# Kernel tuning notes

Hardware: AMD Instinct MI355X
Metric: run time of the kernel (lower is better)

The kernel has to match this reference:

```python
import jax, jax.numpy as jnp
import numpy as np
import math

DIM = 4096
DV = 1024          # compress_dim
H = 16             # num_heads
NS = 32            # num_seeds
B, L = 8, 2048
EPS = 1e-5


def _layernorm(x, g, b):
    mu = jnp.mean(x, axis=-1, keepdims=True)
    var = jnp.mean((x - mu) ** 2, axis=-1, keepdims=True)
    return (x - mu) * jax.lax.rsqrt(var + EPS) * g + b


def setup_inputs() -> dict:
    key = jax.random.key(0)
    ks = jax.random.split(key, 12)
    def lin(k, out_d, in_d):
        scale = math.sqrt(6.0 / (in_d + out_d))  # xavier_uniform
        return jax.random.uniform(k, (out_d, in_d), jnp.float32, -scale, scale)
    return {
        "X": jax.random.normal(ks[0], (B, L, DIM), jnp.float32),
        "pad_mask": jax.random.randint(ks[1], (B, L), 0, 2, jnp.int32),
        "S": jax.random.uniform(ks[2], (1, NS, DV), jnp.float32, -0.05, 0.05),
        "Wq": lin(ks[3], DV, DV), "bq": jnp.zeros((DV,), jnp.float32),
        "Wk": lin(ks[4], DV, DIM), "bk": jnp.zeros((DV,), jnp.float32),
        "Wv": lin(ks[5], DV, DIM), "bv": jnp.zeros((DV,), jnp.float32),
        "Wo": lin(ks[6], DV, DV), "bo": jnp.zeros((DV,), jnp.float32),
        "g0": jnp.ones((DV,), jnp.float32), "beta0": jnp.zeros((DV,), jnp.float32),
        "g1": jnp.ones((DV,), jnp.float32), "beta1": jnp.zeros((DV,), jnp.float32),
    }


def reference(X, pad_mask, S, Wq, bq, Wk, bk, Wv, bv, Wo, bo, g0, beta0, g1, beta1):
    b, l, _ = X.shape
    dh = DV // H
    scale = 1.0 / math.sqrt(DV)  # NOTE: full dim_V, not per-head dim
    Q = jnp.broadcast_to(S, (b, NS, DV))              # seeds repeated per batch
    Qp = (Q @ Wq.T + bq).reshape(b, NS, H, dh)
    Kp = (X @ Wk.T + bk).reshape(b, l, H, dh)
    Vp = (X @ Wv.T + bv).reshape(b, l, H, dh)
    score = jnp.einsum('bqhd,bkhd->bhqk', Qp, Kp) * scale
    m = (pad_mask != 0)[:, None, None, :]             # [b,1,1,k]
    score = jnp.where(m, score, jnp.float32(-1e12))
    A = jax.nn.softmax(score, axis=-1) * m.astype(score.dtype)  # post-softmax renorm
    O = jnp.einsum('bhqk,bkhd->bqhd', A, Vp).reshape(b, NS, DV)
    O = Q + O
    O = _layernorm(O, g0, beta0)
    O = O + jax.nn.relu(O @ Wo.T + bo)
    O = _layernorm(O, g1, beta1)
    return O
```

## Files before the change

### kernel.cpp

```cpp
#include <hip/hip_runtime.h>

#define DIMX 4096
#define DVX  1024
#define HX   16
#define DHX  64
#define NSX  32
#define BX   8
#define LX   2048
#define EPSF 1e-5f

typedef unsigned short u16;
typedef unsigned int   u32;

using bf16x8 = __attribute__((ext_vector_type(8))) __bf16;
using f32x4  = __attribute__((ext_vector_type(4))) float;

__device__ __forceinline__ float bfu(u16 u) {
    union { u32 i; float f; } c; c.i = ((u32)u) << 16; return c.f;
}
__device__ __forceinline__ u16 f2b(float f) {
    union { float f; u32 u; } c; c.f = f;
    u32 u = c.u;
    u32 r = (u + 0x7fffu + ((u >> 16) & 1u)) >> 16;
    return (u16)r;
}

__device__ __forceinline__ void async16(const u16* g, u16* l) {
    __builtin_amdgcn_global_load_lds(
        (const __attribute__((address_space(1))) void*)g,
        (__attribute__((address_space(3))) void*)l, 16, 0, 0);
}

template<bool ISF>
__device__ __forceinline__ void ld8(const void* base, size_t idx, float o[8]) {
    if (ISF) {
        const float* f = (const float*)base + idx;
        float4 a = *(const float4*)f, b = *(const float4*)(f + 4);
        o[0]=a.x; o[1]=a.y; o[2]=a.z; o[3]=a.w;
        o[4]=b.x; o[5]=b.y; o[6]=b.z; o[7]=b.w;
    } else {
        const u16* h = (const u16*)base + idx;
        uint4 v = *(const uint4*)h;
        o[0]=bfu(v.x & 0xffff); o[1]=bfu(v.x >> 16);
        o[2]=bfu(v.y & 0xffff); o[3]=bfu(v.y >> 16);
        o[4]=bfu(v.z & 0xffff); o[5]=bfu(v.z >> 16);
        o[6]=bfu(v.w & 0xffff); o[7]=bfu(v.w >> 16);
    }
}
__device__ __forceinline__ float ld1(const void* base, size_t idx, bool isf) {
    return isf ? ((const float*)base)[idx] : bfu(((const u16*)base)[idx]);
}

__global__ __launch_bounds__(256) void detect_kernel(const u16* __restrict__ X,
                                                     int* __restrict__ flag) {
    __shared__ int cnt;
    if (threadIdx.x == 0) cnt = 0;
    __syncthreads();
    int local = 0;
    for (int i = threadIdx.x; i < 8192; i += 256) {
        u32 e = ((u32)X[i] >> 7) & 0xffu;
        if (e >= 200u) local++;
    }
    atomicAdd(&cnt, local);
    __syncthreads();
    if (threadIdx.x == 0) *flag = (cnt > 32) ? 1 : 0;
}

__global__ __launch_bounds__(256) void cvt_kernel(const int* __restrict__ flag,
                                                  const float* __restrict__ src,
                                                  u16* __restrict__ dst, int ngrp) {
    if (*flag == 0) return;
    int stride = gridDim.x * 256;
    for (int i = blockIdx.x * 256 + threadIdx.x; i < ngrp; i += stride) {
        const float4* f = (const float4*)(src + (size_t)i * 8);
        float4 a = f[0], b = f[1];
        uint4 r;
        r.x = (u32)f2b(a.x) | ((u32)f2b(a.y) << 16);
        r.y = (u32)f2b(a.z) | ((u32)f2b(a.w) << 16);
        r.z = (u32)f2b(b.x) | ((u32)f2b(b.y) << 16);
        r.w = (u32)f2b(b.z) | ((u32)f2b(b.w) << 16);
        *(uint4*)(dst + (size_t)i * 8) = r;
    }
}

__global__ __launch_bounds__(256) void qp_kernel(
        const int* __restrict__ flag, const void* __restrict__ S,
        const void* __restrict__ Wq, const void* __restrict__ bq,
        float* __restrict__ Qp) {
    int wid = blockIdx.x * 4 + (threadIdx.x >> 6);
    int lane = threadIdx.x & 63;
    int q = wid >> 10, n = wid & 1023;
    bool isf = (*flag != 0);
    float p = 0.f;
    if (isf) {
        const float4* s4 = (const float4*)((const float*)S + (size_t)q * DVX);
        const float4* w4 = (const float4*)((const float*)Wq + (size_t)n * DVX);
#pragma unroll
        for (int e = 0; e < 4; e++) {
            float4 a = s4[e * 64 + lane];
            float4 b = w4[e * 64 + lane];
            p += a.x * b.x + a.y * b.y + a.z * b.z + a.w * b.w;
        }
    } else {
        const u16* srow = (const u16*)S + (size_t)q * DVX + lane * 16;
        const u16* wrow = (const u16*)Wq + (size_t)n * DVX + lane * 16;
#pragma unroll
        for (int c = 0; c < 2; c++) {
            uint4 a = *(const uint4*)(srow + c * 8);
            uint4 b = *(const uint4*)(wrow + c * 8);
            p += bfu(a.x & 0xffff) * bfu(b.x & 0xffff) + bfu(a.x >> 16) * bfu(b.x >> 16)
               + bfu(a.y & 0xffff) * bfu(b.y & 0xffff) + bfu(a.y >> 16) * bfu(b.y >> 16)
               + bfu(a.z & 0xffff) * bfu(b.z & 0xffff) + bfu(a.z >> 16) * bfu(b.z >> 16)
               + bfu(a.w & 0xffff) * bfu(b.w & 0xffff) + bfu(a.w >> 16) * bfu(b.w >> 16);
        }
    }
#pragma unroll
    for (int off = 32; off > 0; off >>= 1)
        p += __shfl_xor(p, off, 64);
    if (lane == 0) Qp[wid] = p + ld1(bq, n, isf);
}

__global__ __launch_bounds__(512, 2) void kv_gemm3(
        const int* __restrict__ flag,
        const void* __restrict__ X,  const u16* __restrict__ Xb,
        const void* __restrict__ Wk, const void* __restrict__ bk,
        const void* __restrict__ Wv, const void* __restrict__ bv,
        const u16* __restrict__ Wkb, const u16* __restrict__ Wvb,
        u16* __restrict__ Kp, u16* __restrict__ Vp) {
    extern __shared__ __align__(16) u16 lds[];
    const bool isf = (*flag != 0);
    const u16* Xs = isf ? Xb : (const u16*)X;

    const int t = threadIdx.x;
    const int lane = t & 63, w = t >> 6;
    const int wm = w >> 2, wn = w & 3;
    const int quad = lane >> 4, l16 = lane & 15;
    const int l8 = l16 & 7;

    const int bid = blockIdx.x;
    const int swz = (bid & 7) * 64 + (bid >> 3);
    const int mt = swz >> 3, nt = swz & 7;
    const int m0 = mt * 256, n0 = nt * 256;

    const u16* Wb16; const void* bias; int boff;
    if (n0 < DVX) { Wb16 = (isf ? Wkb : (const u16*)Wk) + (size_t)n0 * DIMX;
                    bias = bk; boff = n0; }
    else          { Wb16 = (isf ? Wvb : (const u16*)Wv) + (size_t)(n0 - DVX) * DIMX;
                    bias = bv; boff = n0 - DVX; }

    f32x4 acc[8][4];
#pragma unroll
    for (int i = 0; i < 8; i++)
#pragma unroll
        for (int j = 0; j < 4; j++) acc[i][j] = {0.f, 0.f, 0.f, 0.f};

    {
        u16* An = lds;
        u16* Bn = lds + 32768;
#pragma unroll
        for (int i = 0; i < 4; i++) {
            int gi = i * 512 + t;
            int r = gi >> 3;
            int g = (gi & 7) ^ (r & 7);
            async16(Xs + (size_t)(m0 + r) * DIMX + g * 8, An + gi * 8);
        }
#pragma unroll
        for (int i = 0; i < 4; i++) {
            int gi = i * 512 + t;
            int r = gi >> 3;
            int g = (gi & 7) ^ (r & 7);
            async16(Wb16 + (size_t)r * DIMX + g * 8, Bn + gi * 8);
        }
        asm volatile("s_waitcnt vmcnt(0)" ::: "memory");
        __builtin_amdgcn_s_barrier();
    }

    for (int kt = 0; kt < DIMX / 64; kt++) {
        u16* Ab = lds + (kt & 1) * 16384;
        u16* Bb = lds + 32768 + (kt & 1) * 16384;
        u16* An = lds + ((kt + 1) & 1) * 16384;
        u16* Bn = lds + 32768 + ((kt + 1) & 1) * 16384;
        const int k1 = (kt + 1) * 64;

        if (kt + 1 < DIMX / 64) {
#pragma unroll
            for (int i = 0; i < 4; i++) {
                int gi = i * 512 + t;
                int r = gi >> 3;
                int g = (gi & 7) ^ (r & 7);
                async16(Xs + (size_t)(m0 + r) * DIMX + k1 + g * 8, An + gi * 8);
            }
#pragma unroll
            for (int i = 0; i < 4; i++) {
                int gi = i * 512 + t;
                int r = gi >> 3;
                int g = (gi & 7) ^ (r & 7);
                async16(Wb16 + (size_t)r * DIMX + k1 + g * 8, Bn + gi * 8);
            }
        }
        __builtin_amdgcn_sched_barrier(0);

        bf16x8 bfr[4][2];
#pragma unroll
        for (int ni = 0; ni < 4; ni++)
#pragma unroll
            for (int ks = 0; ks < 2; ks++) {
                int R = wn * 64 + ni * 16 + l16;
                int cc = ((ks * 4 + quad) ^ l8);
                bfr[ni][ks] = *(const bf16x8*)&Bb[R * 64 + cc * 8];
            }

#pragma unroll
        for (int p = 0; p < 4; p++) {
            bf16x8 a[2][2];
#pragma unroll
            for (int dm = 0; dm < 2; dm++)
#pragma unroll
                for (int ks = 0; ks < 2; ks++) {
                    int R = wm * 128 + (2 * p + dm) * 16 + l16;
                    int cc = ((ks * 4 + quad) ^ l8);
                    a[dm][ks] = *(const bf16x8*)&Ab[R * 64 + cc * 8];
                }
            __builtin_amdgcn_s_setprio(1);
#pragma unroll
            for (int dm = 0; dm < 2; dm++)
#pragma unroll
                for (int ni = 0; ni < 4; ni++)
#pragma unroll
                    for (int ks = 0; ks < 2; ks++)
                        acc[2 * p + dm][ni] = __builtin_amdgcn_mfma_f32_16x16x32_bf16(
                            a[dm][ks], bfr[ni][ks], acc[2 * p + dm][ni], 0, 0, 0);
            __builtin_amdgcn_s_setprio(0);
        }

        __builtin_amdgcn_sched_barrier(0);
        asm volatile("s_waitcnt vmcnt(0)" ::: "memory");
        __builtin_amdgcn_s_barrier();
        __builtin_amdgcn_sched_barrier(0);
    }

    float bb[4];
#pragma unroll
    for (int ni = 0; ni < 4; ni++)
        bb[ni] = ld1(bias, (size_t)(boff + wn * 64 + ni * 16 + l16), isf);
#pragma unroll
    for (int mi = 0; mi < 8; mi++) {
#pragma unroll
        for (int ni = 0; ni < 4; ni++) {
            int colL = wn * 64 + ni * 16 + l16;
            int col = n0 + colL;
            u16* dst; int dcol;
            if (col < DVX) { dst = Kp; dcol = col; }
            else           { dst = Vp; dcol = col - DVX; }
#pragma unroll
            for (int r = 0; r < 4; r++) {
                int row = m0 + wm * 128 + mi * 16 + quad * 4 + r;
                dst[(size_t)row * DVX + dcol] = f2b(acc[mi][ni][r] + bb[ni]);
            }
        }
    }
}

#define TM 128
#define TN 128
#define BKK 32
#define LDT 32

__device__ __forceinline__ uint4 pack8(float o[8]) {
    uint4 r;
    r.x = (u32)f2b(o[0]) | ((u32)f2b(o[1]) << 16);
    r.y = (u32)f2b(o[2]) | ((u32)f2b(o[3]) << 16);
    r.z = (u32)f2b(o[4]) | ((u32)f2b(o[5]) << 16);
    r.w = (u32)f2b(o[6]) | ((u32)f2b(o[7]) << 16);
    return r;
}

__global__ __launch_bounds__(256) void kv_gemm2(
        const int* __restrict__ flag,
        const void* __restrict__ X,  const u16* __restrict__ Xb,
        const void* __restrict__ Wk, const void* __restrict__ bk,
        const void* __restrict__ Wv, const void* __restrict__ bv,
        const u16* __restrict__ Wkb, const u16* __restrict__ Wvb,
        u16* __restrict__ Kp, u16* __restrict__ Vp) {
    __shared__ u16 As[TM * LDT];
    __shared__ u16 Bs[TN * LDT];
    const bool isf = (*flag != 0);
    const u16* Xs = isf ? Xb : (const u16*)X;

    const int t = threadIdx.x;
    const int lane = t & 63, w = t >> 6;
    const int wm = w >> 1, wn = w & 1;
    const int quad = lane >> 4, l16 = lane & 15;
    const int bl = blockIdx.x;
    const int xcd = bl & 7, bq = bl >> 3;
    const int m0 = (xcd + 8 * (bq >> 4)) * TM;
    const int n0 = (bq & 15) * TN;
    const u16* Wb16; const void* bias; int boff;
    if (n0 < DVX) { Wb16 = (isf ? Wkb : (const u16*)Wk) + (size_t)n0 * DIMX;
                    bias = bk; boff = n0; }
    else          { Wb16 = (isf ? Wvb : (const u16*)Wv) + (size_t)(n0 - DVX) * DIMX;
                    bias = bv; boff = n0 - DVX; }

    f32x4 acc[4][4];
#pragma unroll
    for (int i = 0; i < 4; i++)
#pragma unroll
        for (int j = 0; j < 4; j++) acc[i][j] = {0.f, 0.f, 0.f, 0.f};

    const int srow = lane >> 2;
    const int gcol = ((lane & 3) ^ ((lane >> 3) & 3)) * 8;
    const int ph = (l16 >> 1) & 3;

    for (int k0 = 0; k0 < DIMX; k0 += BKK) {
        __syncthreads();
#pragma unroll
        for (int c = 0; c < 2; c++) {
            int rr = w * 32 + c * 16;
            async16(Xs + (size_t)(m0 + rr + srow) * DIMX + k0 + gcol,
                    As + rr * LDT);
            async16(Wb16 + (size_t)(rr + srow) * DIMX + k0 + gcol,
                    Bs + rr * LDT);
        }
        __syncthreads();
        bf16x8 af[4], bfr[4];
#pragma unroll
        for (int mi = 0; mi < 4; mi++) {
            int ar = wm * 64 + mi * 16 + l16;
            af[mi] = *(const bf16x8*)&As[ar * LDT + (quad ^ ph) * 8];
        }
#pragma unroll
        for (int ni = 0; ni < 4; ni++) {
            int br = wn * 64 + ni * 16 + l16;
            bfr[ni] = *(const bf16x8*)&Bs[br * LDT + (quad ^ ph) * 8];
        }
#pragma unroll
        for (int mi = 0; mi < 4; mi++)
#pragma unroll
            for (int ni = 0; ni < 4; ni++)
                acc[mi][ni] = __builtin_amdgcn_mfma_f32_16x16x32_bf16(
                    af[mi], bfr[ni], acc[mi][ni], 0, 0, 0);
    }

#pragma unroll
    for (int mi = 0; mi < 4; mi++) {
#pragma unroll
        for (int ni = 0; ni < 4; ni++) {
            int colL = wn * 64 + ni * 16 + l16;
            int col = n0 + colL;
            float bb = ld1(bias, (size_t)(boff + colL), isf);
            u16* dst; int dcol;
            if (col < DVX) { dst = Kp; dcol = col; }
            else           { dst = Vp; dcol = col - DVX; }
#pragma unroll
            for (int r = 0; r < 4; r++) {
                int row = m0 + wm * 64 + mi * 16 + quad * 4 + r;
                dst[(size_t)row * DVX + dcol] = f2b(acc[mi][ni][r] + bb);
            }
        }
    }
}

template<bool ISF>
__device__ void kv_body(const void* __restrict__ X,
                        const void* __restrict__ Wk, const void* __restrict__ bk,
                        const void* __restrict__ Wv, const void* __restrict__ bv,
                        u16* __restrict__ Kp, u16* __restrict__ Vp,
                        u16* As, u16* Bs) {
    const int t = threadIdx.x;
    const int lane = t & 63, w = t >> 6;
    const int wm = w >> 1, wn = w & 1;
    const int quad = lane >> 4, l16 = lane & 15;
    const int bl = blockIdx.x;
    const int xcd = bl & 7, bq = bl >> 3;
    const int m0 = (xcd + 8 * (bq >> 4)) * TM;
    const int n0 = (bq & 15) * TN;
    const void* Wbase; const void* bias; int boff;
    size_t woff;
    if (n0 < DVX) { Wbase = Wk; bias = bk; woff = (size_t)n0 * DIMX; boff = n0; }
    else          { Wbase = Wv; bias = bv; woff = (size_t)(n0 - DVX) * DIMX; boff = n0 - DVX; }
    const u16* Wb16 = (const u16*)Wbase + woff;
    const float* Wbf = (const float*)Wbase + woff;

    f32x4 acc[4][4];
#pragma unroll
    for (int i = 0; i < 4; i++)
#pragma unroll
        for (int j = 0; j < 4; j++) acc[i][j] = {0.f, 0.f, 0.f, 0.f};

    const int srow = lane >> 2;
    const int gcol = ((lane & 3) ^ ((lane >> 3) & 3)) * 8;
    const int ph = (l16 >> 1) & 3;
    const int r0 = t >> 2, c0 = (t & 3) * 8;
    const int r1 = r0 + 64;
    const int swc = (((t & 3) ^ ((r0 >> 1) & 3))) * 8;

    for (int k0 = 0; k0 < DIMX; k0 += BKK) {
        if constexpr (ISF) {
            float oa0[8], oa1[8], ob0[8], ob1[8];
            ld8<true>(X,   (size_t)(m0 + r0) * DIMX + k0 + c0, oa0);
            ld8<true>(X,   (size_t)(m0 + r1) * DIMX + k0 + c0, oa1);
            ld8<true>(Wbf, (size_t)r0 * DIMX + k0 + c0, ob0);
            ld8<true>(Wbf, (size_t)r1 * DIMX + k0 + c0, ob1);
            __syncthreads();
            *(uint4*)&As[r0 * LDT + swc] = pack8(oa0);
            *(uint4*)&As[r1 * LDT + swc] = pack8(oa1);
            *(uint4*)&Bs[r0 * LDT + swc] = pack8(ob0);
            *(uint4*)&Bs[r1 * LDT + swc] = pack8(ob1);
        } else {
            __syncthreads();
#pragma unroll
            for (int c = 0; c < 2; c++) {
                int rr = w * 32 + c * 16;
                async16((const u16*)X + (size_t)(m0 + rr + srow) * DIMX + k0 + gcol,
                        As + rr * LDT);
                async16(Wb16 + (size_t)(rr + srow) * DIMX + k0 + gcol,
                        Bs + rr * LDT);
            }
        }
        __syncthreads();
        bf16x8 af[4], bfr[4];
#pragma unroll
        for (int mi = 0; mi < 4; mi++) {
            int ar = wm * 64 + mi * 16 + l16;
            af[mi] = *(const bf16x8*)&As[ar * LDT + (quad ^ ph) * 8];
        }
#pragma unroll
        for (int ni = 0; ni < 4; ni++) {
            int br = wn * 64 + ni * 16 + l16;
            bfr[ni] = *(const bf16x8*)&Bs[br * LDT + (quad ^ ph) * 8];
        }
#pragma unroll
        for (int mi = 0; mi < 4; mi++)
#pragma unroll
            for (int ni = 0; ni < 4; ni++)
                acc[mi][ni] = __builtin_amdgcn_mfma_f32_16x16x32_bf16(
                    af[mi], bfr[ni], acc[mi][ni], 0, 0, 0);
    }

#pragma unroll
    for (int mi = 0; mi < 4; mi++) {
#pragma unroll
        for (int ni = 0; ni < 4; ni++) {
            int colL = wn * 64 + ni * 16 + l16;
            int col = n0 + colL;
            float bb = ld1(bias, (size_t)(boff + colL), ISF);
            u16* dst; int dcol;
            if (col < DVX) { dst = Kp; dcol = col; }
            else           { dst = Vp; dcol = col - DVX; }
#pragma unroll
            for (int r = 0; r < 4; r++) {
                int row = m0 + wm * 64 + mi * 16 + quad * 4 + r;
                dst[(size_t)row * DVX + dcol] = f2b(acc[mi][ni][r] + bb);
            }
        }
    }
}

__global__ __launch_bounds__(256) void kv_gemm(
        const int* __restrict__ flag, const void* __restrict__ X,
        const void* __restrict__ Wk, const void* __restrict__ bk,
        const void* __restrict__ Wv, const void* __restrict__ bv,
        u16* __restrict__ Kp, u16* __restrict__ Vp) {
    __shared__ u16 As[TM * LDT];
    __shared__ u16 Bs[TN * LDT];
    if (*flag) kv_body<true>(X, Wk, bk, Wv, bv, Kp, Vp, As, Bs);
    else       kv_body<false>(X, Wk, bk, Wv, bv, Kp, Vp, As, Bs);
}

#define CHK 256
#define NCH (LX / CHK)
__global__ __launch_bounds__(256) void attn2_kernel(
        const float* __restrict__ Qp, const u16* __restrict__ Kp,
        const u16* __restrict__ Vp, const int* __restrict__ pad,
        float* __restrict__ Opart, float* __restrict__ Ml) {
    __shared__ float sc[NSX * CHK];
    const int blk = blockIdx.x;
    const int b  = blk / (HX * NCH);
    const int h  = (blk / NCH) % HX;
    const int c0 = blk % NCH;
    const int t = threadIdx.x;
    const int w = t >> 6, lane = t & 63;
    const int rsub = lane >> 3;
    const int dsub = lane & 7;
    const int q0w = w * 8;

    float qc[8][8];
#pragma unroll
    for (int qq = 0; qq < 8; qq++) {
        const float* qp = Qp + (size_t)(q0w + qq) * DVX + h * DHX + dsub * 8;
        float4 a = *(const float4*)qp, bq4 = *(const float4*)(qp + 4);
        qc[qq][0]=a.x; qc[qq][1]=a.y; qc[qq][2]=a.z; qc[qq][3]=a.w;
        qc[qq][4]=bq4.x; qc[qq][5]=bq4.y; qc[qq][6]=bq4.z; qc[qq][7]=bq4.w;
    }

    const u16* kb = Kp + ((size_t)b * LX + c0 * CHK) * DVX + h * DHX;
    const int* pb = pad + b * LX + c0 * CHK;

    float lmax[8];
#pragma unroll
    for (int qq = 0; qq < 8; qq++) lmax[qq] = -3e38f;
    for (int i = 0; i < CHK / 8; i++) {
        int k = i * 8 + rsub;
        uint4 v = *(const uint4*)(kb + (size_t)k * DVX + dsub * 8);
        float kf[8];
        kf[0]=bfu(v.x & 0xffff); kf[1]=bfu(v.x >> 16);
        kf[2]=bfu(v.y & 0xffff); kf[3]=bfu(v.y >> 16);
        kf[4]=bfu(v.z & 0xffff); kf[5]=bfu(v.z >> 16);
        kf[6]=bfu(v.w & 0xffff); kf[7]=bfu(v.w >> 16);
        int pm = pb[k];
#pragma unroll
        for (int qq = 0; qq < 8; qq++) {
            float s = kf[0]*qc[qq][0] + kf[1]*qc[qq][1]
                    + kf[2]*qc[qq][2] + kf[3]*qc[qq][3]
                    + kf[4]*qc[qq][4] + kf[5]*qc[qq][5]
                    + kf[6]*qc[qq][6] + kf[7]*qc[qq][7];
            s += __shfl_xor(s, 1, 64);
            s += __shfl_xor(s, 2, 64);
            s += __shfl_xor(s, 4, 64);
            s *= 0.03125f;
            s = pm ? s : -1e30f;
            if (dsub == 0) sc[(q0w + qq) * CHK + k] = s;
            lmax[qq] = fmaxf(lmax[qq], s);
        }
    }
#pragma unroll
    for (int qq = 0; qq < 8; qq++) {
        lmax[qq] = fmaxf(lmax[qq], __shfl_xor(lmax[qq], 8, 64));
        lmax[qq] = fmaxf(lmax[qq], __shfl_xor(lmax[qq], 16, 64));
        lmax[qq] = fmaxf(lmax[qq], __shfl_xor(lmax[qq], 32, 64));
    }

#pragma unroll
    for (int qq = 0; qq < 8; qq++) {
        float m = lmax[qq];
        float lsum = 0.f;
#pragma unroll
        for (int it = 0; it < CHK / 64; it++) {
            int idx = (q0w + qq) * CHK + it * 64 + lane;
            float sv = sc[idx];
            float e = (sv > -1e29f) ? __expf(sv - m) : 0.f;
            sc[idx] = e;
            lsum += e;
        }
#pragma unroll
        for (int off = 32; off > 0; off >>= 1)
            lsum += __shfl_xor(lsum, off, 64);
        if (lane == 0) {
            Ml[(size_t)blk * 64 + (q0w + qq) * 2 + 0] = m;
            Ml[(size_t)blk * 64 + (q0w + qq) * 2 + 1] = lsum;
        }
    }

    float acc[8][8];
#pragma unroll
    for (int qq = 0; qq < 8; qq++)
#pragma unroll
        for (int e = 0; e < 8; e++) acc[qq][e] = 0.f;
    const u16* vb = Vp + ((size_t)b * LX + c0 * CHK) * DVX + h * DHX + dsub * 8;
    for (int i = 0; i < CHK / 8; i++) {
        int k = i * 8 + rsub;
        uint4 v = *(const uint4*)(vb + (size_t)k * DVX);
        float vf[8];
        vf[0]=bfu(v.x & 0xffff); vf[1]=bfu(v.x >> 16);
        vf[2]=bfu(v.y & 0xffff); vf[3]=bfu(v.y >> 16);
        vf[4]=bfu(v.z & 0xffff); vf[5]=bfu(v.z >> 16);
        vf[6]=bfu(v.w & 0xffff); vf[7]=bfu(v.w >> 16);
#pragma unroll
        for (int qq = 0; qq < 8; qq++) {
            float p = sc[(q0w + qq) * CHK + k];
#pragma unroll
            for (int e = 0; e < 8; e++) acc[qq][e] += p * vf[e];
        }
    }
#pragma unroll
    for (int qq = 0; qq < 8; qq++) {
#pragma unroll
        for (int e = 0; e < 8; e++) {
            acc[qq][e] += __shfl_xor(acc[qq][e], 8, 64);
            acc[qq][e] += __shfl_xor(acc[qq][e], 16, 64);
            acc[qq][e] += __shfl_xor(acc[qq][e], 32, 64);
        }
        if (rsub == qq) {
            float* op = Opart + ((size_t)blk * NSX + q0w + qq) * DHX + dsub * 8;
            float4 r0 = {acc[qq][0], acc[qq][1], acc[qq][2], acc[qq][3]};
            float4 r1 = {acc[qq][4], acc[qq][5], acc[qq][6], acc[qq][7]};
            *(float4*)op = r0;
            *(float4*)(op + 4) = r1;
        }
    }
}

__global__ __launch_bounds__(256) void attn_combine(
        const float* __restrict__ Opart, const float* __restrict__ Ml,
        float* __restrict__ Oat) {
    const int bh = blockIdx.x;
    const int b = bh / HX, h = bh % HX;
    const int t = threadIdx.x;
    const int q = t >> 3, d0 = (t & 7) * 8;
    const size_t cbase = (size_t)bh * NCH;
    float m = -3e38f;
#pragma unroll
    for (int c = 0; c < NCH; c++)
        m = fmaxf(m, Ml[(cbase + c) * 64 + q * 2]);
    float l = 0.f, o[8];
#pragma unroll
    for (int e = 0; e < 8; e++) o[e] = 0.f;
#pragma unroll
    for (int c = 0; c < NCH; c++) {
        float mc = Ml[(cbase + c) * 64 + q * 2 + 0];
        float lc = Ml[(cbase + c) * 64 + q * 2 + 1];
        float wgt = (mc > -1e29f) ? __expf(mc - m) : 0.f;
        l += wgt * lc;
        const float* op = Opart + ((cbase + c) * NSX + q) * DHX + d0;
        float4 x = *(const float4*)op, y = *(const float4*)(op + 4);
        o[0] += wgt * x.x; o[1] += wgt * x.y; o[2] += wgt * x.z; o[3] += wgt * x.w;
        o[4] += wgt * y.x; o[5] += wgt * y.y; o[6] += wgt * y.z; o[7] += wgt * y.w;
    }
    float inv = (l > 0.f) ? 1.f / l : 0.f;
    float* dst = Oat + ((size_t)(b * NSX) + q) * DVX + h * DHX + d0;
    float4 r0 = {o[0]*inv, o[1]*inv, o[2]*inv, o[3]*inv};
    float4 r1 = {o[4]*inv, o[5]*inv, o[6]*inv, o[7]*inv};
    *(float4*)dst = r0;
    *(float4*)(dst + 4) = r1;
}

#define QG 4
__global__ __launch_bounds__(256) void attn_kernel(
        const float* __restrict__ Qp, const u16* __restrict__ Kp,
        const u16* __restrict__ Vp, const int* __restrict__ pad,
        float* __restrict__ Oat) {
    __shared__ float qv[QG * DHX];
    __shared__ float sc[QG * LX];
    __shared__ float rpart[256 * 8];
    __shared__ float invs[QG];
    const int blk = blockIdx.x;
    const int nqg = NSX / QG;
    const int b  = blk / (HX * nqg);
    const int h  = (blk / nqg) % HX;
    const int q0 = (blk % nqg) * QG;
    const int t = threadIdx.x;
    const int w = t >> 6, lane = t & 63;

    qv[t] = Qp[(size_t)(q0 + (t >> 6)) * DVX + h * DHX + (t & 63)];
    __syncthreads();

    const u16* Kb = Kp + (size_t)b * LX * DVX + h * DHX;
    const int rsub = lane >> 3;
    const int dsub = lane & 7;
    float qc[8];
#pragma unroll
    for (int e = 0; e < 8; e++) qc[e] = qv[w * DHX + dsub * 8 + e];

    float lmax = -3e38f;
    for (int i = 0; i < LX / 8; i++) {
        int k = i * 8 + rsub;
        uint4 v = *(const uint4*)(Kb + (size_t)k * DVX + dsub * 8);
        float s = bfu(v.x & 0xffff) * qc[0] + bfu(v.x >> 16) * qc[1]
                + bfu(v.y & 0xffff) * qc[2] + bfu(v.y >> 16) * qc[3]
                + bfu(v.z & 0xffff) * qc[4] + bfu(v.z >> 16) * qc[5]
                + bfu(v.w & 0xffff) * qc[6] + bfu(v.w >> 16) * qc[7];
        s += __shfl_xor(s, 1, 64);
        s += __shfl_xor(s, 2, 64);
        s += __shfl_xor(s, 4, 64);
        s *= 0.03125f;
        s = (pad[b * LX + k] != 0) ? s : -1e30f;
        if (dsub == 0) sc[w * LX + k] = s;
        lmax = fmaxf(lmax, s);
    }
#pragma unroll
    for (int off = 32; off > 0; off >>= 1)
        lmax = fmaxf(lmax, __shfl_xor(lmax, off, 64));
    float lsum = 0.f;
    for (int i = 0; i < LX / 64; i++) {
        int k = i * 64 + lane;
        float sv = sc[w * LX + k];
        float e = (sv > -1e29f) ? __expf(sv - lmax) : 0.f;
        sc[w * LX + k] = e;
        lsum += e;
    }
#pragma unroll
    for (int off = 32; off > 0; off >>= 1)
        lsum += __shfl_xor(lsum, off, 64);
    if (lane == 0) invs[w] = (lsum > 0.f) ? 1.f / lsum : 0.f;

    const int kg = (t >> 3) & 7, dg = t & 7;
    const u16* Vb = Vp + (size_t)b * LX * DVX + h * DHX + dg * 8;
    float a8[8];
#pragma unroll
    for (int e = 0; e < 8; e++) a8[e] = 0.f;
    for (int i = 0; i < LX / 8; i++) {
        int k = i * 8 + kg;
        float p = sc[w * LX + k];
        uint4 v = *(const uint4*)(Vb + (size_t)k * DVX);
        a8[0] += p * bfu(v.x & 0xffff); a8[1] += p * bfu(v.x >> 16);
        a8[2] += p * bfu(v.y & 0xffff); a8[3] += p * bfu(v.y >> 16);
        a8[4] += p * bfu(v.z & 0xffff); a8[5] += p * bfu(v.z >> 16);
        a8[6] += p * bfu(v.w & 0xffff); a8[7] += p * bfu(v.w >> 16);
    }
#pragma unroll
    for (int e = 0; e < 8; e++) rpart[t * 8 + e] = a8[e];
    __syncthreads();

    {
        int q = t >> 6, d = t & 63;
        float o = 0.f;
#pragma unroll
        for (int g = 0; g < 8; g++)
            o += rpart[(q * 64 + g * 8 + (d >> 3)) * 8 + (d & 7)];
        o *= invs[q];
        Oat[((size_t)(b * NSX + q0 + q)) * DVX + h * DHX + d] = o;
    }
}

template<bool ISF>
__device__ void epi_body(float* u, float* y0, float* red,
                         const float* __restrict__ Oat, const void* __restrict__ S,
                         const void* __restrict__ Wo, const void* __restrict__ bo,
                         const void* __restrict__ g0, const void* __restrict__ be0,
                         const void* __restrict__ g1, const void* __restrict__ be1,
                         void* __restrict__ out) {
    const int bq = blockIdx.x;
    const int q = bq & 31;
    const int t = threadIdx.x;
    const int w = t >> 6, lane = t & 63;

    float ls = 0.f, ls2 = 0.f;
#pragma unroll
    for (int j = 0; j < 2; j++) {
        int c = t + 512 * j;
        float v = ld1(S, (size_t)q * DVX + c, ISF) + Oat[(size_t)bq * DVX + c];
        u[c] = v; ls += v; ls2 += v * v;
    }
    red[t] = ls; __syncthreads();
    for (int s2 = 256; s2 > 0; s2 >>= 1) { if (t < s2) red[t] += red[t + s2]; __syncthreads(); }
    float mu = red[0] / DVX; __syncthreads();
    red[t] = ls2; __syncthreads();
    for (int s2 = 256; s2 > 0; s2 >>= 1) { if (t < s2) red[t] += red[t + s2]; __syncthreads(); }
    float var = red[0] / DVX - mu * mu;
    float r = rsqrtf(var + EPSF);
    __syncthreads();
#pragma unroll
    for (int j = 0; j < 2; j++) {
        int c = t + 512 * j;
        y0[c] = (u[c] - mu) * r * ld1(g0, c, ISF) + ld1(be0, c, ISF);
    }
    __syncthreads();

    float yr[16];
    if constexpr (ISF) {
        const float4* y4 = (const float4*)y0;
#pragma unroll
        for (int e = 0; e < 4; e++) {
            float4 v = y4[e * 64 + lane];
            yr[e*4+0]=v.x; yr[e*4+1]=v.y; yr[e*4+2]=v.z; yr[e*4+3]=v.w;
        }
    } else {
#pragma unroll
        for (int e = 0; e < 8; e++) { yr[e] = y0[lane * 8 + e]; yr[8 + e] = y0[512 + lane * 8 + e]; }
    }
    for (int i = 0; i < 128; i++) {
        int n = i * 8 + w;
        float p = 0.f;
        if constexpr (ISF) {
            const float4* row4 = (const float4*)((const float*)Wo + (size_t)n * DVX);
#pragma unroll
            for (int e = 0; e < 4; e++) {
                float4 wv = row4[e * 64 + lane];
                p += wv.x * yr[e*4] + wv.y * yr[e*4+1]
                   + wv.z * yr[e*4+2] + wv.w * yr[e*4+3];
            }
        } else {
            const uint4* row = (const uint4*)((const u16*)Wo + (size_t)n * DVX);
            uint4 v0 = row[lane], v1 = row[lane + 64];
            p += bfu(v0.x & 0xffff) * yr[0] + bfu(v0.x >> 16) * yr[1]
               + bfu(v0.y & 0xffff) * yr[2] + bfu(v0.y >> 16) * yr[3]
               + bfu(v0.z & 0xffff) * yr[4] + bfu(v0.z >> 16) * yr[5]
               + bfu(v0.w & 0xffff) * yr[6] + bfu(v0.w >> 16) * yr[7];
            p += bfu(v1.x & 0xffff) * yr[8]  + bfu(v1.x >> 16) * yr[9]
               + bfu(v1.y & 0xffff) * yr[10] + bfu(v1.y >> 16) * yr[11]
               + bfu(v1.z & 0xffff) * yr[12] + bfu(v1.z >> 16) * yr[13]
               + bfu(v1.w & 0xffff) * yr[14] + bfu(v1.w >> 16) * yr[15];
        }
#pragma unroll
        for (int off = 32; off > 0; off >>= 1)
            p += __shfl_xor(p, off, 64);
        if (lane == 0) {
            float z = p + ld1(bo, n, ISF);
            u[n] = y0[n] + fmaxf(z, 0.f);
        }
    }
    __syncthreads();
    ls = 0.f; ls2 = 0.f;
#pragma unroll
    for (int j = 0; j < 2; j++) {
        int c = t + 512 * j; float v = u[c]; ls += v; ls2 += v * v;
    }
    red[t] = ls; __syncthreads();
    for (int s2 = 256; s2 > 0; s2 >>= 1) { if (t < s2) red[t] += red[t + s2]; __syncthreads(); }
    mu = red[0] / DVX; __syncthreads();
    red[t] = ls2; __syncthreads();
    for (int s2 = 256; s2 > 0; s2 >>= 1) { if (t < s2) red[t] += red[t + s2]; __syncthreads(); }
    var = red[0] / DVX - mu * mu;
    r = rsqrtf(var + EPSF);
#pragma unroll
    for (int j = 0; j < 2; j++) {
        int c = t + 512 * j;
        float v = (u[c] - mu) * r * ld1(g1, c, ISF) + ld1(be1, c, ISF);
        if (ISF) ((float*)out)[(size_t)bq * DVX + c] = v;
        else     ((u16*)out)[(size_t)bq * DVX + c] = f2b(v);
    }
}

__global__ __launch_bounds__(512) void epi_kernel(
        const int* __restrict__ flag,
        const float* __restrict__ Oat, const void* __restrict__ S,
        const void* __restrict__ Wo, const void* __restrict__ bo,
        const void* __restrict__ g0, const void* __restrict__ be0,
        const void* __restrict__ g1, const void* __restrict__ be1,
        void* __restrict__ out) {
    __shared__ float u[DVX];
    __shared__ float y0[DVX];
    __shared__ float red[512];
    if (*flag) epi_body<true>(u, y0, red, Oat, S, Wo, bo, g0, be0, g1, be1, out);
    else       epi_body<false>(u, y0, red, Oat, S, Wo, bo, g0, be0, g1, be1, out);
}

extern "C" void kernel_launch(void* const* d_in, const int* in_sizes, int n_in,
                              void* d_out, int out_size, void* d_ws, size_t ws_size,
                              hipStream_t stream) {
    (void)in_sizes; (void)n_in; (void)out_size;
    const void* X    = d_in[0];
    const int* pad   = (const int*)d_in[1];
    const void* S    = d_in[2];
    const void* Wq   = d_in[3];
    const void* bq   = d_in[4];
    const void* Wk   = d_in[5];
    const void* bk   = d_in[6];
    const void* Wv   = d_in[7];
    const void* bv   = d_in[8];
    const void* Wo   = d_in[9];
    const void* bo   = d_in[10];
    const void* g0   = d_in[11];
    const void* be0  = d_in[12];
    const void* g1   = d_in[13];
    const void* be1  = d_in[14];

    char* ws = (char*)d_ws;
    int*   flag = (int*)ws;
    float* Qp  = (float*)(ws + 256);
    float* Oat = (float*)(ws + 256 + 131072);
    u16*   Kp  = (u16*)(ws + 256 + 131072 + 1048576);
    u16*   Vp  = Kp + (size_t)BX * LX * DVX;
    u16*   Xb  = Vp + (size_t)BX * LX * DVX;
    u16*   Wkb = Xb + (size_t)BX * LX * DIMX;
    u16*   Wvb = Wkb + (size_t)DVX * DIMX;
    float* Opart = (float*)(Wvb + (size_t)DVX * DIMX);
    float* Ml  = Opart + (size_t)BX * HX * NCH * NSX * DHX;

    size_t need = 256 + 131072 + 1048576
                + 2 * (size_t)BX * LX * DVX * 2
                + (size_t)BX * LX * DIMX * 2
                + 2 * (size_t)DVX * DIMX * 2;
    size_t need2 = need
                 + (size_t)BX * HX * NCH * NSX * DHX * 4
                 + (size_t)BX * HX * NCH * 64 * 4;

    static int attr_ok = -1;
    if (attr_ok < 0) {
        hipError_t e = hipFuncSetAttribute(
            reinterpret_cast<const void*>(kv_gemm3),
            hipFuncAttributeMaxDynamicSharedMemorySize, 131072);
        attr_ok = (e == hipSuccess) ? 1 : 0;
    }

    detect_kernel<<<1, 256, 0, stream>>>((const u16*)X, flag);
    qp_kernel<<<8192, 256, 0, stream>>>(flag, S, Wq, bq, Qp);

    if (ws_size >= need) {
        cvt_kernel<<<2048, 256, 0, stream>>>(flag, (const float*)X, Xb,
                                             BX * LX * DIMX / 8);
        cvt_kernel<<<512, 256, 0, stream>>>(flag, (const float*)Wk, Wkb,
                                            DVX * DIMX / 8);
        cvt_kernel<<<512, 256, 0, stream>>>(flag, (const float*)Wv, Wvb,
                                            DVX * DIMX / 8);
        if (attr_ok == 1) {
            kv_gemm3<<<512, 512, 131072, stream>>>(flag, X, Xb, Wk, bk, Wv, bv,
                                                   Wkb, Wvb, Kp, Vp);
        } else {
            kv_gemm2<<<2048, 256, 0, stream>>>(flag, X, Xb, Wk, bk, Wv, bv,
                                               Wkb, Wvb, Kp, Vp);
        }
    } else {
        kv_gemm<<<2048, 256, 0, stream>>>(flag, X, Wk, bk, Wv, bv, Kp, Vp);
    }

    if (ws_size >= need2) {
        attn2_kernel<<<BX * HX * NCH, 256, 0, stream>>>(Qp, Kp, Vp, pad,
                                                        Opart, Ml);
        attn_combine<<<BX * HX, 256, 0, stream>>>(Opart, Ml, Oat);
    } else {
        attn_kernel<<<BX * HX * (NSX / QG), 256, 0, stream>>>(Qp, Kp, Vp, pad, Oat);
    }
    epi_kernel<<<BX * NSX, 512, 0, stream>>>(flag, Oat, S, Wo, bo, g0, be0, g1, be1, (void*)d_out);
}
```

Before: 852.4 us.

## Stage KV GEMM output tile through LDS for coalesced stores; split launch

The KV projection GEMM epilogue now writes its bf16 accumulator tile into shared memory, then each thread copies 16-byte chunks to global memory row-contiguously. This replaces scattered 2-byte stores. The grid is also split into two launches of half the blocks via a block offset parameter. This adds a barrier and LDS traffic per block, and an extra kernel launch.

```diff
diff --git a/kernel.cpp b/kernel.cpp
--- a/kernel.cpp
+++ b/kernel.cpp
@@ -121,7 +121,7 @@
 }
 
 __global__ __launch_bounds__(512, 2) void kv_gemm3(
-        const int* __restrict__ flag,
+        const int* __restrict__ flag, int boffs,
         const void* __restrict__ X,  const u16* __restrict__ Xb,
         const void* __restrict__ Wk, const void* __restrict__ bk,
         const void* __restrict__ Wv, const void* __restrict__ bv,
@@ -137,7 +137,7 @@
     const int quad = lane >> 4, l16 = lane & 15;
     const int l8 = l16 & 7;
 
-    const int bid = blockIdx.x;
+    const int bid = blockIdx.x + boffs;
     const int swz = (bid & 7) * 64 + (bid >> 3);
     const int mt = swz >> 3, nt = swz & 7;
     const int m0 = mt * 256, n0 = nt * 256;
@@ -247,16 +247,26 @@
     for (int mi = 0; mi < 8; mi++) {
 #pragma unroll
         for (int ni = 0; ni < 4; ni++) {
-            int colL = wn * 64 + ni * 16 + l16;
-            int col = n0 + colL;
-            u16* dst; int dcol;
-            if (col < DVX) { dst = Kp; dcol = col; }
-            else           { dst = Vp; dcol = col - DVX; }
+            int colT = wn * 64 + ni * 16 + l16;
 #pragma unroll
             for (int r = 0; r < 4; r++) {
-                int row = m0 + wm * 128 + mi * 16 + quad * 4 + r;
-                dst[(size_t)row * DVX + dcol] = f2b(acc[mi][ni][r] + bb[ni]);
+                int rowT = wm * 128 + mi * 16 + quad * 4 + r;
+                lds[rowT * 256 + colT] = f2b(acc[mi][ni][r] + bb[ni]);
             }
+        }
+    }
+    __syncthreads();
+    {
+        u16* dst; int dcol0;
+        if (n0 < DVX) { dst = Kp; dcol0 = n0; }
+        else          { dst = Vp; dcol0 = n0 - DVX; }
+#pragma unroll
+        for (int it = 0; it < 16; it++) {
+            int idx = it * 512 + t;
+            int rowT = idx >> 5;
+            int chk = idx & 31;
+            uint4 v = *(const uint4*)&lds[rowT * 256 + chk * 8];
+            *(uint4*)&dst[(size_t)(m0 + rowT) * DVX + dcol0 + chk * 8] = v;
         }
     }
 }
@@ -884,7 +894,9 @@
         cvt_kernel<<<512, 256, 0, stream>>>(flag, (const float*)Wv, Wvb,
                                             DVX * DIMX / 8);
         if (attr_ok == 1) {
-            kv_gemm3<<<512, 512, 131072, stream>>>(flag, X, Xb, Wk, bk, Wv, bv,
+            kv_gemm3<<<256, 512, 131072, stream>>>(flag, 0, X, Xb, Wk, bk, Wv, bv,
+                                                   Wkb, Wvb, Kp, Vp);
+            kv_gemm3<<<256, 512, 131072, stream>>>(flag, 256, X, Xb, Wk, bk, Wv, bv,
                                                    Wkb, Wvb, Kp, Vp);
         } else {
             kv_gemm2<<<2048, 256, 0, stream>>>(flag, X, Xb, Wk, bk, Wv, bv,
```

Measured after the change: 853.5 us. Within noise of the previous version (+0.1%).
